# Performance work log

Hardware: AMD Instinct MI355X
Metric: run time of the kernel (lower is better)

Reference implementation:

```python
import jax, jax.numpy as jnp
import numpy as np

NEG_INF = -9e15  # mask value used by the original module
LEAKY_SLOPE = 0.2


def setup_inputs() -> dict:
    key = jax.random.key(0)
    k1, k2, k3, k4 = jax.random.split(key, 4)
    B, N, F_in = 4, 2048, 128
    H, head_dim = 4, 32
    h = jax.random.normal(k1, (B, N, F_in), dtype=jnp.float32)
    adj = jax.random.randint(k2, (N, N), 0, 2, dtype=jnp.int32)
    W = jax.random.normal(k3, (H, F_in, head_dim), dtype=jnp.float32)
    a = jax.random.normal(k4, (H, 2 * head_dim, 1), dtype=jnp.float32)
    return {"h": h, "adj": adj, "W": W, "a": a}


def reference(h, adj, W, a):
    # h: (B, N, F_in); adj: (N, N) int; W: (H, F_in, D); a: (H, 2D, 1)
    D = W.shape[-1]
    Wh = jnp.einsum('bnf,hfd->bhnd', h, W)          # (B, H, N, D)
    # Original builds [Wh_i || Wh_j] @ a. Split a so that
    # e_ij = Wh_i . a_src + Wh_j . a_dst  (identical math, no N^2*2D concat).
    a_src = a[:, :D, 0]                              # (H, D)
    a_dst = a[:, D:, 0]                              # (H, D)
    e_src = jnp.einsum('bhnd,hd->bhn', Wh, a_src)    # (B, H, N)
    e_dst = jnp.einsum('bhnd,hd->bhn', Wh, a_dst)    # (B, H, N)
    e = jax.nn.leaky_relu(e_src[..., :, None] + e_dst[..., None, :],
                          negative_slope=LEAKY_SLOPE)  # (B, H, N, N)
    masked = jnp.where(adj[None, None] > 0, e, NEG_INF)
    attn = jax.nn.softmax(masked, axis=-1)           # dropout: eval mode (identity)
    out = jnp.einsum('bhij,bhjd->bhid', attn, Wh)    # (B, H, N, D)
    B, H, N, _ = out.shape
    # concat heads along feature dim == transpose to (B, N, H, D) then merge
    return out.transpose(0, 2, 1, 3).reshape(B, N, H * D)
```

## Files before the change

### kernel.cpp

```cpp
#include <hip/hip_runtime.h>
#include <hip/hip_bf16.h>

typedef unsigned short u16;
using f32x4 = __attribute__((ext_vector_type(4))) float;
using short8 = __attribute__((ext_vector_type(8))) short;

constexpr int B_ = 4, N_ = 2048, FIN = 128, H_ = 4, D_ = 32;
constexpr int BH = B_ * H_;
constexpr float LOG2E = 1.4426950408889634f;

constexpr int NPB = 16;

__global__ __launch_bounds__(256) void wh_kernel(
    const float* __restrict__ h, const float* __restrict__ W,
    const float* __restrict__ a, u16* __restrict__ WhT,
    float* __restrict__ es, float* __restrict__ ed) {
  __shared__ float hsh[NPB][FIN];
  __shared__ float part[NPB][H_][D_];
  const int t = threadIdx.x;
  const int fh = t >> 7, hh = (t >> 5) & 3, d = t & 31;

  float Wr[64];
#pragma unroll
  for (int ff = 0; ff < 64; ++ff)
    Wr[ff] = W[hh * (FIN * D_) + (fh * 64 + ff) * D_ + d];

  const int n0 = blockIdx.x * NPB;
  for (int idx = t; idx < NPB * FIN; idx += 256)
    hsh[idx >> 7][idx & 127] = h[(size_t)n0 * FIN + idx];
  __syncthreads();

  float accs[NPB];
#pragma unroll
  for (int r = 0; r < NPB; ++r) {
    float acc = 0.f;
    const float* hr = &hsh[r][fh * 64];
#pragma unroll
    for (int f4 = 0; f4 < 16; ++f4) {
      float4 hv = *(const float4*)(hr + f4 * 4);
      acc += hv.x * Wr[f4 * 4 + 0];
      acc += hv.y * Wr[f4 * 4 + 1];
      acc += hv.z * Wr[f4 * 4 + 2];
      acc += hv.w * Wr[f4 * 4 + 3];
    }
    accs[r] = acc;
  }
  if (fh == 0) {
#pragma unroll
    for (int r = 0; r < NPB; ++r) part[r][hh][d] = accs[r];
  }
  __syncthreads();
  if (fh == 1) {
    const int b = n0 / N_;
    const int bh = b * H_ + hh;
    const int n0r = n0 & (N_ - 1);
    const float asrc = a[hh * 2 * D_ + d];
    const float adst = a[hh * 2 * D_ + D_ + d];
    union { u16 s[16]; uint4 q[2]; } wbuf;
#pragma unroll
    for (int r = 0; r < NPB; ++r) {
      const float wh = accs[r] + part[r][hh][d];
      union { __hip_bfloat16 h; u16 u; } cv;
      cv.h = __float2bfloat16(wh);
      wbuf.s[r] = cv.u;
      float vs = wh * asrc, vd = wh * adst;
#pragma unroll
      for (int o = 16; o >= 1; o >>= 1) {
        vs += __shfl_xor(vs, o, 64);
        vd += __shfl_xor(vd, o, 64);
      }
      if (d == 0) {
        es[(size_t)bh * N_ + n0r + r] = vs * LOG2E;
        ed[(size_t)bh * N_ + n0r + r] = vd * LOG2E;
      }
    }
    u16* dst = WhT + ((size_t)(bh * 32 + d)) * N_ + n0r;
    *(uint4*)dst = wbuf.q[0];
    *(uint4*)(dst + 8) = wbuf.q[1];
  }
}

__global__ __launch_bounds__(256) void pack_kernel(
    const int* __restrict__ adj, unsigned long long* __restrict__ mask) {
  const int gid = blockIdx.x * 256 + threadIdx.x;
  const int wdx = gid >> 6;
  const int lane = threadIdx.x & 63;
  const int i = wdx >> 5;
  const int jb = (wdx & 31) << 6;
  const int v = adj[(size_t)i * N_ + jb + lane];
  const unsigned long long m = __ballot(v > 0);
  if (lane == 0) mask[wdx] = m;
}

constexpr int ROWS = 32;
constexpr int NSTEP = 32;

__global__ __launch_bounds__(256) void attn_kernel(
    const float* __restrict__ es, const float* __restrict__ ed,
    const u16* __restrict__ WhT, const unsigned int* __restrict__ mask32,
    float* __restrict__ out) {
  __shared__ __align__(16) char arena[16640];
  __shared__ float essh[ROWS], rmsh[ROWS];

  float* edsh = (float*)arena;
  unsigned int* maskw = (unsigned int*)(arena + 8192);
  unsigned char* maskb = (unsigned char*)(arena + 8192);

  const int bh = blockIdx.x >> 6;
  const int i0 = (blockIdx.x & 63) * ROWS;
  const int tid = threadIdx.x, lane = tid & 63, w = tid >> 6;
  const int tile = w & 1, jh = w >> 1;

  const float* edb = ed + (size_t)bh * N_;
  *(float4*)&edsh[tid * 8] = *(const float4*)(edb + tid * 8);
  *(float4*)&edsh[tid * 8 + 4] = *(const float4*)(edb + tid * 8 + 4);
  const unsigned int* mrow = mask32 + (size_t)i0 * 64;
#pragma unroll
  for (int q = 0; q < 8; ++q) {
    const int idx = tid + q * 256;
    maskw[(idx >> 6) * 65 + (idx & 63)] = mrow[(idx >> 6) * 64 + (idx & 63)];
  }
  if (tid < ROWS) essh[tid] = es[(size_t)bh * N_ + i0 + tid];
  __syncthreads();

#pragma unroll
  for (int q8 = 0; q8 < 8; ++q8) {
    const int r = w * 8 + q8;
    float mx = -3.0e38f;
#pragma unroll
    for (int q = 0; q < 32; ++q) {
      const unsigned int mword = maskw[r * 65 + q * 2 + (lane >> 5)];
      const float v = edsh[q * 64 + lane];
      mx = ((mword >> (lane & 31)) & 1u) ? fmaxf(mx, v) : mx;
    }
#pragma unroll
    for (int o = 32; o >= 1; o >>= 1) mx = fmaxf(mx, __shfl_xor(mx, o, 64));
    if (lane == 0) rmsh[r] = mx;
  }
  __syncthreads();

  const int row16 = lane & 15, kg = lane >> 4;
  const int row32 = tile * 16 + row16;
  const float esr = essh[row32];
  const float xm = esr + rmsh[row32];
  const float mxr = fmaxf(xm, 0.2f * xm);

  const u16* wb0 = WhT + ((size_t)(bh * 32 + row16)) * N_ + jh * 1024 + kg * 8;
  const u16* wb1 = wb0 + (size_t)16 * N_;

  f32x4 c0 = {}, c1 = {};
  float sum = 0.f;
  short8 b0 = *(const short8*)wb0;
  short8 b1 = *(const short8*)wb1;

  for (int s = 0; s < NSTEP; ++s) {
    const int sn = (s + 1 < NSTEP) ? (s + 1) : (NSTEP - 1);
    const short8 nb0 = *(const short8*)(wb0 + sn * 32);
    const short8 nb1 = *(const short8*)(wb1 + sn * 32);

    const int k0 = jh * 1024 + s * 32;
    const unsigned int mb = maskb[row32 * 260 + (k0 >> 3) + kg];
    const float4 ea = *(const float4*)&edsh[k0 + kg * 8];
    const float4 eb = *(const float4*)&edsh[k0 + kg * 8 + 4];
    const float ev[8] = {ea.x, ea.y, ea.z, ea.w, eb.x, eb.y, eb.z, eb.w};
    float p[8];
#pragma unroll
    for (int j = 0; j < 8; ++j) {
      const float x = esr + ev[j];
      const float y = fmaxf(x, 0.2f * x);
      float z = fminf(y - mxr, 0.f);
      z = (mb & (1u << j)) ? z : -1e30f;
      p[j] = exp2f(z);
      sum += p[j];
    }
    union { unsigned int u[4]; short8 v8; } af;
    asm("v_cvt_pk_bf16_f32 %0, %1, %2" : "=v"(af.u[0]) : "v"(p[0]), "v"(p[1]));
    asm("v_cvt_pk_bf16_f32 %0, %1, %2" : "=v"(af.u[1]) : "v"(p[2]), "v"(p[3]));
    asm("v_cvt_pk_bf16_f32 %0, %1, %2" : "=v"(af.u[2]) : "v"(p[4]), "v"(p[5]));
    asm("v_cvt_pk_bf16_f32 %0, %1, %2" : "=v"(af.u[3]) : "v"(p[6]), "v"(p[7]));

    c0 = __builtin_amdgcn_mfma_f32_16x16x32_bf16(af.v8, b0, c0, 0, 0, 0);
    c1 = __builtin_amdgcn_mfma_f32_16x16x32_bf16(af.v8, b1, c1, 0, 0, 0);
    b0 = nb0;
    b1 = nb1;
  }

  __syncthreads();

  float* redc = (float*)arena;
  float* sumsh = (float*)(arena + 16384);
  sum += __shfl_xor(sum, 16, 64);
  sum += __shfl_xor(sum, 32, 64);
  if (lane < 16) sumsh[(tile * 2 + jh) * 16 + lane] = sum;
#pragma unroll
  for (int r = 0; r < 4; ++r) {
    redc[(((tile * 2 + jh) * 16) + kg * 4 + r) * 32 + row16] = c0[r];
    redc[(((tile * 2 + jh) * 16) + kg * 4 + r) * 32 + 16 + row16] = c1[r];
  }
  __syncthreads();

  const int r32 = tid >> 3;
  const int c4 = (tid & 7) * 4;
  const int tl = r32 >> 4, rr = r32 & 15;
  const float inv =
      1.f / fmaxf(sumsh[(tl * 2 + 0) * 16 + rr] + sumsh[(tl * 2 + 1) * 16 + rr],
                  1e-30f);
  const float* r0 = &redc[((tl * 2 + 0) * 16 + rr) * 32 + c4];
  const float* r1 = &redc[((tl * 2 + 1) * 16 + rr) * 32 + c4];
  float4 o;
  o.x = (r0[0] + r1[0]) * inv;
  o.y = (r0[1] + r1[1]) * inv;
  o.z = (r0[2] + r1[2]) * inv;
  o.w = (r0[3] + r1[3]) * inv;
  const int b = bh >> 2, hh = bh & 3;
  *(float4*)&out[((size_t)(b * N_ + i0 + r32)) * (H_ * D_) + hh * 32 + c4] = o;
}

extern "C" void kernel_launch(void* const* d_in, const int* in_sizes, int n_in,
                              void* d_out, int out_size, void* d_ws,
                              size_t ws_size, hipStream_t stream) {
  const float* h = (const float*)d_in[0];
  const int* adj = (const int*)d_in[1];
  const float* W = (const float*)d_in[2];
  const float* a = (const float*)d_in[3];
  char* ws = (char*)d_ws;
  u16* WhT = (u16*)ws;
  float* es = (float*)(ws + (2u << 20));
  float* ed = (float*)(ws + (2u << 20) + (128u << 10));
  unsigned long long* mask =
      (unsigned long long*)(ws + (2u << 20) + (256u << 10));
  float* out = (float*)d_out;

  wh_kernel<<<B_ * N_ / NPB, 256, 0, stream>>>(h, W, a, WhT, es, ed);
  pack_kernel<<<N_ * N_ / 256, 256, 0, stream>>>(adj, mask);
  attn_kernel<<<BH * (N_ / ROWS), 256, 0, stream>>>(
      es, ed, WhT, (const unsigned int*)mask, out);
}
```

Measured before the change: 145.0 us.

## Split attention rows into 16-row blocks with 4-way key split and MFMA row sums

The attention kernel now handles 16 query rows per block instead of 32. Each of the four waves covers a quarter of the key range for all 16 rows, which doubles the grid size and adds an occupancy hint to the launch bounds. The softmax denominator now comes from an extra MFMA against a ones vector, replacing the scalar adds and shuffles. The leaky-relu exponent is rewritten as a select between two precomputed affine forms. In exchange, each block loads the full ed vector per 16 rows and performs a 4-way cross-wave reduction through shared memory.

```diff
diff --git a/kernel.cpp b/kernel.cpp
--- a/kernel.cpp
+++ b/kernel.cpp
@@ -92,31 +92,32 @@
   if (lane == 0) mask[wdx] = m;
 }
 
-constexpr int ROWS = 32;
-constexpr int NSTEP = 32;
-
-__global__ __launch_bounds__(256) void attn_kernel(
+constexpr int ROWS = 16;
+constexpr int NSTEP = 16;
+
+__global__ __launch_bounds__(256, 6) void attn_kernel(
     const float* __restrict__ es, const float* __restrict__ ed,
     const u16* __restrict__ WhT, const unsigned int* __restrict__ mask32,
     float* __restrict__ out) {
-  __shared__ __align__(16) char arena[16640];
+  __shared__ __align__(16) char arena[12352];
   __shared__ float essh[ROWS], rmsh[ROWS];
+  __shared__ float sumsh[4][16];
 
   float* edsh = (float*)arena;
   unsigned int* maskw = (unsigned int*)(arena + 8192);
   unsigned char* maskb = (unsigned char*)(arena + 8192);
 
-  const int bh = blockIdx.x >> 6;
-  const int i0 = (blockIdx.x & 63) * ROWS;
+  const int bh = blockIdx.x >> 7;
+  const int i0 = (blockIdx.x & 127) * ROWS;
   const int tid = threadIdx.x, lane = tid & 63, w = tid >> 6;
-  const int tile = w & 1, jh = w >> 1;
+  const int jq = w;
 
   const float* edb = ed + (size_t)bh * N_;
   *(float4*)&edsh[tid * 8] = *(const float4*)(edb + tid * 8);
   *(float4*)&edsh[tid * 8 + 4] = *(const float4*)(edb + tid * 8 + 4);
   const unsigned int* mrow = mask32 + (size_t)i0 * 64;
 #pragma unroll
-  for (int q = 0; q < 8; ++q) {
+  for (int q = 0; q < 4; ++q) {
     const int idx = tid + q * 256;
     maskw[(idx >> 6) * 65 + (idx & 63)] = mrow[(idx >> 6) * 64 + (idx & 63)];
   }
@@ -124,8 +125,8 @@
   __syncthreads();
 
 #pragma unroll
-  for (int q8 = 0; q8 < 8; ++q8) {
-    const int r = w * 8 + q8;
+  for (int q4 = 0; q4 < 4; ++q4) {
+    const int r = w * 4 + q4;
     float mx = -3.0e38f;
 #pragma unroll
     for (int q = 0; q < 32; ++q) {
@@ -140,16 +141,21 @@
   __syncthreads();
 
   const int row16 = lane & 15, kg = lane >> 4;
-  const int row32 = tile * 16 + row16;
-  const float esr = essh[row32];
-  const float xm = esr + rmsh[row32];
+  const float esr = essh[row16];
+  const float xm = esr + rmsh[row16];
   const float mxr = fmaxf(xm, 0.2f * xm);
-
-  const u16* wb0 = WhT + ((size_t)(bh * 32 + row16)) * N_ + jh * 1024 + kg * 8;
+  const float cpos = esr - mxr;
+  const float cneg = 0.2f * esr - mxr;
+  const float thr = -esr;
+
+  const u16* wb0 = WhT + ((size_t)(bh * 32 + row16)) * N_ + jq * 512 + kg * 8;
   const u16* wb1 = wb0 + (size_t)16 * N_;
 
-  f32x4 c0 = {}, c1 = {};
-  float sum = 0.f;
+  short8 ones;
+#pragma unroll
+  for (int q = 0; q < 8; ++q) ones[q] = (short)0x3F80;
+
+  f32x4 c0 = {}, c1 = {}, csum = {};
   short8 b0 = *(const short8*)wb0;
   short8 b1 = *(const short8*)wb1;
 
@@ -158,20 +164,20 @@
     const short8 nb0 = *(const short8*)(wb0 + sn * 32);
     const short8 nb1 = *(const short8*)(wb1 + sn * 32);
 
-    const int k0 = jh * 1024 + s * 32;
-    const unsigned int mb = maskb[row32 * 260 + (k0 >> 3) + kg];
+    const int k0 = jq * 512 + s * 32;
+    const unsigned int mb = maskb[row16 * 260 + (k0 >> 3) + kg];
     const float4 ea = *(const float4*)&edsh[k0 + kg * 8];
     const float4 eb = *(const float4*)&edsh[k0 + kg * 8 + 4];
     const float ev[8] = {ea.x, ea.y, ea.z, ea.w, eb.x, eb.y, eb.z, eb.w};
     float p[8];
 #pragma unroll
     for (int j = 0; j < 8; ++j) {
-      const float x = esr + ev[j];
-      const float y = fmaxf(x, 0.2f * x);
-      float z = fminf(y - mxr, 0.f);
+      const float edv = ev[j];
+      const float zp = edv + cpos;
+      const float zn = __builtin_fmaf(edv, 0.2f, cneg);
+      float z = (edv >= thr) ? zp : zn;
       z = (mb & (1u << j)) ? z : -1e30f;
       p[j] = exp2f(z);
-      sum += p[j];
     }
     union { unsigned int u[4]; short8 v8; } af;
     asm("v_cvt_pk_bf16_f32 %0, %1, %2" : "=v"(af.u[0]) : "v"(p[0]), "v"(p[1]));
@@ -181,6 +187,7 @@
 
     c0 = __builtin_amdgcn_mfma_f32_16x16x32_bf16(af.v8, b0, c0, 0, 0, 0);
     c1 = __builtin_amdgcn_mfma_f32_16x16x32_bf16(af.v8, b1, c1, 0, 0, 0);
+    csum = __builtin_amdgcn_mfma_f32_16x16x32_bf16(af.v8, ones, csum, 0, 0, 0);
     b0 = nb0;
     b1 = nb1;
   }
@@ -188,32 +195,35 @@
   __syncthreads();
 
   float* redc = (float*)arena;
-  float* sumsh = (float*)(arena + 16384);
-  sum += __shfl_xor(sum, 16, 64);
-  sum += __shfl_xor(sum, 32, 64);
-  if (lane < 16) sumsh[(tile * 2 + jh) * 16 + lane] = sum;
 #pragma unroll
   for (int r = 0; r < 4; ++r) {
-    redc[(((tile * 2 + jh) * 16) + kg * 4 + r) * 32 + row16] = c0[r];
-    redc[(((tile * 2 + jh) * 16) + kg * 4 + r) * 32 + 16 + row16] = c1[r];
-  }
-  __syncthreads();
-
-  const int r32 = tid >> 3;
-  const int c4 = (tid & 7) * 4;
-  const int tl = r32 >> 4, rr = r32 & 15;
-  const float inv =
-      1.f / fmaxf(sumsh[(tl * 2 + 0) * 16 + rr] + sumsh[(tl * 2 + 1) * 16 + rr],
-                  1e-30f);
-  const float* r0 = &redc[((tl * 2 + 0) * 16 + rr) * 32 + c4];
-  const float* r1 = &redc[((tl * 2 + 1) * 16 + rr) * 32 + c4];
-  float4 o;
-  o.x = (r0[0] + r1[0]) * inv;
-  o.y = (r0[1] + r1[1]) * inv;
-  o.z = (r0[2] + r1[2]) * inv;
-  o.w = (r0[3] + r1[3]) * inv;
-  const int b = bh >> 2, hh = bh & 3;
-  *(float4*)&out[((size_t)(b * N_ + i0 + r32)) * (H_ * D_) + hh * 32 + c4] = o;
+    redc[(jq * 16 + kg * 4 + r) * 33 + row16] = c0[r];
+    redc[(jq * 16 + kg * 4 + r) * 33 + 16 + row16] = c1[r];
+  }
+  if (row16 == 0) {
+#pragma unroll
+    for (int r = 0; r < 4; ++r) sumsh[jq][kg * 4 + r] = csum[r];
+  }
+  __syncthreads();
+
+  if (tid < 128) {
+    const int r = tid >> 3;
+    const int c4 = (tid & 7) * 4;
+    const float inv =
+        1.f / fmaxf(sumsh[0][r] + sumsh[1][r] + sumsh[2][r] + sumsh[3][r],
+                    1e-30f);
+    float4 o;
+    const float* p0 = &redc[(0 * 16 + r) * 33 + c4];
+    const float* p1 = &redc[(1 * 16 + r) * 33 + c4];
+    const float* p2 = &redc[(2 * 16 + r) * 33 + c4];
+    const float* p3 = &redc[(3 * 16 + r) * 33 + c4];
+    o.x = (p0[0] + p1[0] + p2[0] + p3[0]) * inv;
+    o.y = (p0[1] + p1[1] + p2[1] + p3[1]) * inv;
+    o.z = (p0[2] + p1[2] + p2[2] + p3[2]) * inv;
+    o.w = (p0[3] + p1[3] + p2[3] + p3[3]) * inv;
+    const int b = bh >> 2, hh = bh & 3;
+    *(float4*)&out[((size_t)(b * N_ + i0 + r)) * (H_ * D_) + hh * 32 + c4] = o;
+  }
 }
 
 extern "C" void kernel_launch(void* const* d_in, const int* in_sizes, int n_in,
```

After: 133.8 us. 1.08x faster.
